# Kernel optimization log

Measured on AMD Instinct MI355X. Metric: run time of the kernel, lower is better.

The kernel has to match this reference:

```python
import jax, jax.numpy as jnp
import numpy as np

B, T, CODE_NUM, MED_NUM = 256, 32, 4880, 1000
CODE_SIZE, H, OUT = 128, 128, 4880


def setup_inputs() -> dict:
    key = jax.random.key(0)
    ks = jax.random.split(key, 16)
    code_x = (jax.random.uniform(ks[0], (B, T, CODE_NUM)) < 0.05).astype(jnp.float32)
    medicine_codes = (jax.random.uniform(ks[1], (B, T, MED_NUM)) < 0.02).astype(jnp.float32)
    divided = (jax.random.uniform(ks[2], (B, T, CODE_NUM)) < 0.05).astype(jnp.float32)
    neighbors = (jax.random.uniform(ks[3], (B, T, CODE_NUM)) < 0.05).astype(jnp.float32)
    lens = jax.random.randint(ks[4], (B,), 1, T + 1)
    s = lambda fan: 1.0 / np.sqrt(fan)
    c_emb = jax.random.normal(ks[5], (CODE_NUM, CODE_SIZE)) * s(CODE_SIZE)
    m_emb = jax.random.normal(ks[6], (MED_NUM, CODE_SIZE)) * s(CODE_SIZE)
    W_c = jax.random.normal(ks[7], (CODE_SIZE, H)) * s(CODE_SIZE)
    W_m = jax.random.normal(ks[8], (CODE_SIZE, H)) * s(CODE_SIZE)
    Wa = jax.random.normal(ks[9], (3 * H, 32)) * s(3 * H)
    ba = jnp.zeros((32,), jnp.float32)
    va = jax.random.normal(ks[10], (32,)) * s(32)
    W_cls = jax.random.normal(ks[11], (3 * H, OUT)) * s(3 * H)
    b_cls = jnp.zeros((OUT,), jnp.float32)
    return dict(code_x=code_x, divided=divided, neighbors=neighbors, lens=lens,
                medicine_codes=medicine_codes, c_emb=c_emb, m_emb=m_emb,
                W_c=W_c, W_m=W_m, Wa=Wa, ba=ba, va=va, W_cls=W_cls, b_cls=b_cls)


def _forward(code_x, medicine_codes, lens, c_emb, m_emb, W_c, W_m, Wa, ba, va, W_cls, b_cls):
    # hypergraph_part: transform code/med embeddings, aggregate active codes per visit
    Hc = jnp.tanh(c_emb @ W_c)                      # [code_num, H]
    Hm = jnp.tanh(m_emb @ W_m)                      # [med_num, H]
    sum_c = jnp.einsum('btc,ch->bth', code_x, Hc)   # masked sum over active dx codes
    sum_m = jnp.einsum('btm,mh->bth', medicine_codes, Hm)
    h_c = sum_c / jnp.clip(code_x.sum(-1, keepdims=True), 1.0, None)
    h_m = sum_m / jnp.clip(medicine_codes.sum(-1, keepdims=True), 1.0, None)
    repre = jnp.concatenate([h_c, h_m, h_c * h_m], axis=-1)  # [B,T,3H]
    # DotProductAttention over visits, masked by lens
    scores = jnp.einsum('btk,k->bt', jnp.tanh(repre @ Wa + ba), va)
    mask = jnp.arange(T)[None, :] < lens[:, None]
    attn = jax.nn.softmax(jnp.where(mask, scores, -1e9), axis=-1)
    ctx = jnp.einsum('bt,btd->bd', attn, repre)     # [B,3H]
    # Classifier (dropout=identity in eval) + sigmoid
    return jax.nn.sigmoid(ctx @ W_cls + b_cls)      # [B,OUT]


def reference(code_x, divided, neighbors, lens, medicine_codes, c_emb, m_emb,
              W_c, W_m, Wa, ba, va, W_cls, b_cls):
    # divided/neighbors feed the transition branch whose output is unused
    # in the original forward's final prediction path.
    return _forward(code_x, medicine_codes, lens, c_emb, m_emb,
                    W_c, W_m, Wa, ba, va, W_cls, b_cls)
```

## Files before the change

### kernel.cpp

```cpp
#include <hip/hip_runtime.h>
#include <hip/hip_bf16.h>
#include <math.h>

#define Bsz 256
#define Tn 32
#define CODEN 4880
#define MEDN 1000
#define Hdim 128
#define OUTN 4880
#define R3H 384
#define NROW (Bsz * Tn)
#define NC4 (CODEN / 4)
#define NM4 (MEDN / 4)
#define CCAP 384
#define MCAP 64
#define CROWS (CODEN + 8)
#define MROWS (MEDN + 8)

typedef unsigned short u16;
typedef unsigned int u32;
typedef __attribute__((ext_vector_type(4))) float f32x4;

__device__ inline int mbcnt64(unsigned long long m) {
  return __builtin_amdgcn_mbcnt_hi((u32)(m >> 32),
         __builtin_amdgcn_mbcnt_lo((u32)m, 0));
}
__device__ inline u32 f2bf(float f) {
  u32 u = __float_as_uint(f);
  return (u + 0x7fffu + ((u >> 16) & 1u)) >> 16;
}

__global__ __launch_bounds__(128) void k_emb(
    const float* __restrict__ c_emb, const float* __restrict__ m_emb,
    const float* __restrict__ W_c, const float* __restrict__ W_m,
    u32* __restrict__ Hc2, u32* __restrict__ Hm2) {
  int blk = blockIdx.x, h = threadIdx.x;
  bool is_med = blk >= CROWS;
  int c = is_med ? blk - CROWS : blk;
  int n = is_med ? MEDN : CODEN;
  u32* out2 = (is_med ? Hm2 + (size_t)c * 64 : Hc2 + (size_t)c * 64);
  if (c >= n) { if ((h & 1) == 0) out2[h >> 1] = 0; return; }
  const float* emb = (is_med ? m_emb : c_emb) + (size_t)c * Hdim;
  const float* W = is_med ? W_m : W_c;
  __shared__ float e[Hdim];
  e[h] = emb[h];
  __syncthreads();
  float acc = 0.f;
#pragma unroll 8
  for (int k = 0; k < Hdim; ++k) acc += e[k] * W[k * Hdim + h];
  float vme = tanhf(acc);
  float vnx = __shfl_down(vme, 1, 64);
  if ((h & 1) == 0) out2[h >> 1] = f2bf(vme) | (f2bf(vnx) << 16);
}

__global__ __launch_bounds__(256) void k_pack(
    const float* __restrict__ code_x, const float* __restrict__ med,
    u16* __restrict__ idx_c, u16* __restrict__ idx_m,
    int* __restrict__ cnt_c, int* __restrict__ cnt_m) {
  int v = blockIdx.x, tid = threadIdx.x, lane = tid & 63;
  __shared__ u16 lc[CCAP + 8];
  __shared__ u16 lm[MCAP + 8];
  __shared__ int cc, cm;
  if (tid == 0) { cc = 0; cm = 0; }
  __syncthreads();

  const float4* cx = (const float4*)(code_x + (size_t)v * CODEN);
  const float4* mx = (const float4*)(med + (size_t)v * MEDN);
  float4 x[5], xm;
#pragma unroll
  for (int it = 0; it < 5; ++it) {
    int i = it * 256 + tid;
    x[it] = (i < NC4) ? cx[i] : make_float4(0.f, 0.f, 0.f, 0.f);
  }
  xm = (tid < NM4) ? mx[tid] : make_float4(0.f, 0.f, 0.f, 0.f);

#pragma unroll
  for (int it = 0; it < 5; ++it) {
    int i = it * 256 + tid;
    float4 vv = x[it];
    unsigned long long m0 = __ballot(vv.x != 0.f);
    unsigned long long m1 = __ballot(vv.y != 0.f);
    unsigned long long m2 = __ballot(vv.z != 0.f);
    unsigned long long m3 = __ballot(vv.w != 0.f);
    int c0 = __popcll(m0), c1 = __popcll(m1), c2 = __popcll(m2), c3 = __popcll(m3);
    int base = 0;
    if (lane == 0) base = atomicAdd(&cc, c0 + c1 + c2 + c3);
    base = __builtin_amdgcn_readfirstlane(base);
    int p;
    p = base + mbcnt64(m0);             if (vv.x != 0.f && p < CCAP) lc[p] = (u16)(4 * i);
    p = base + c0 + mbcnt64(m1);        if (vv.y != 0.f && p < CCAP) lc[p] = (u16)(4 * i + 1);
    p = base + c0 + c1 + mbcnt64(m2);   if (vv.z != 0.f && p < CCAP) lc[p] = (u16)(4 * i + 2);
    p = base + c0 + c1 + c2 + mbcnt64(m3); if (vv.w != 0.f && p < CCAP) lc[p] = (u16)(4 * i + 3);
  }
  {
    int i = tid;
    unsigned long long m0 = __ballot(xm.x != 0.f);
    unsigned long long m1 = __ballot(xm.y != 0.f);
    unsigned long long m2 = __ballot(xm.z != 0.f);
    unsigned long long m3 = __ballot(xm.w != 0.f);
    int c0 = __popcll(m0), c1 = __popcll(m1), c2 = __popcll(m2), c3 = __popcll(m3);
    int base = 0;
    if (lane == 0) base = atomicAdd(&cm, c0 + c1 + c2 + c3);
    base = __builtin_amdgcn_readfirstlane(base);
    int p;
    p = base + mbcnt64(m0);             if (xm.x != 0.f && p < MCAP) lm[p] = (u16)(4 * i);
    p = base + c0 + mbcnt64(m1);        if (xm.y != 0.f && p < MCAP) lm[p] = (u16)(4 * i + 1);
    p = base + c0 + c1 + mbcnt64(m2);   if (xm.z != 0.f && p < MCAP) lm[p] = (u16)(4 * i + 2);
    p = base + c0 + c1 + c2 + mbcnt64(m3); if (xm.w != 0.f && p < MCAP) lm[p] = (u16)(4 * i + 3);
  }
  __syncthreads();
  int nc = cc < CCAP ? cc : CCAP;
  int nm = cm < MCAP ? cm : MCAP;
  int ncp = (nc + 7) & ~7, nmp = (nm + 7) & ~7;
  for (int i = nc + tid; i < ncp; i += 256) lc[i] = (u16)CODEN;
  for (int i = nm + tid; i < nmp; i += 256) lm[i] = (u16)MEDN;
  __syncthreads();
  u32* gc = (u32*)(idx_c + (size_t)v * CCAP);
  for (int i = tid; i < (ncp >> 1); i += 256) gc[i] = ((const u32*)lc)[i];
  u32* gm = (u32*)(idx_m + (size_t)v * MCAP);
  if (tid < (nmp >> 1)) gm[tid] = ((const u32*)lm)[tid];
  if (tid == 0) { cnt_c[v] = nc; cnt_m[v] = nm; }
}

__global__ __launch_bounds__(256) void k_gather(
    const u16* __restrict__ idx_c, const u16* __restrict__ idx_m,
    const int* __restrict__ cnt_c, const int* __restrict__ cnt_m,
    const u32* __restrict__ Hc2, const u32* __restrict__ Hm2,
    u32* __restrict__ rep2) {
  __shared__ u16 slc[4][CCAP];
  __shared__ u16 slm[4][MCAP];
  int tid = threadIdx.x;
  int w = tid >> 6, l = tid & 63;
  int v = blockIdx.x * 4 + w;
  int nc = cnt_c[v], nm = cnt_m[v];
  int ncp = (nc + 7) & ~7, nmp = (nm + 7) & ~7;

  {
    const u32* gc = (const u32*)(idx_c + (size_t)v * CCAP);
    u32* d = (u32*)slc[w];
    for (int i = l; i < (ncp >> 1); i += 64) d[i] = gc[i];
    const u32* gm = (const u32*)(idx_m + (size_t)v * MCAP);
    u32* dm = (u32*)slm[w];
    if (l < (nmp >> 1)) dm[l] = gm[l];
  }
  __syncthreads();

  float a0 = 0.f, a1 = 0.f;
  const u32* lcu = (const u32*)slc[w];
  for (int j = 0; j < ncp; j += 8) {
    u32 pr[4], vv[8];
#pragma unroll
    for (int u = 0; u < 4; ++u) pr[u] = lcu[(j >> 1) + u];
#pragma unroll
    for (int u = 0; u < 4; ++u) {
      vv[2 * u]     = Hc2[(size_t)(pr[u] & 0xffffu) * 64 + l];
      vv[2 * u + 1] = Hc2[(size_t)(pr[u] >> 16) * 64 + l];
    }
#pragma unroll
    for (int u = 0; u < 8; ++u) {
      a0 += __uint_as_float(vv[u] << 16);
      a1 += __uint_as_float(vv[u] & 0xffff0000u);
    }
  }
  float m0 = 0.f, m1 = 0.f;
  const u32* lmu = (const u32*)slm[w];
  for (int j = 0; j < nmp; j += 8) {
    u32 pr[4], vv[8];
#pragma unroll
    for (int u = 0; u < 4; ++u) pr[u] = lmu[(j >> 1) + u];
#pragma unroll
    for (int u = 0; u < 4; ++u) {
      vv[2 * u]     = Hm2[(size_t)(pr[u] & 0xffffu) * 64 + l];
      vv[2 * u + 1] = Hm2[(size_t)(pr[u] >> 16) * 64 + l];
    }
#pragma unroll
    for (int u = 0; u < 8; ++u) {
      m0 += __uint_as_float(vv[u] << 16);
      m1 += __uint_as_float(vv[u] & 0xffff0000u);
    }
  }
  float ic = 1.f / fmaxf((float)nc, 1.f);
  float im = 1.f / fmaxf((float)nm, 1.f);
  rep2[(size_t)v * 128 + l]      = f2bf(a0 * ic) | (f2bf(a1 * ic) << 16);
  rep2[(size_t)v * 128 + 64 + l] = f2bf(m0 * im) | (f2bf(m1 * im) << 16);
}

__global__ __launch_bounds__(256) void k_post(
    const u32* __restrict__ rep2, const float* __restrict__ Wa,
    const float* __restrict__ ba, const float* __restrict__ va,
    const int* __restrict__ lens, float* __restrict__ ctx) {
  __shared__ float rep_s[Tn][R3H + 4];
  __shared__ float sc_s[Tn];
  __shared__ float at_s[Tn];
  int b = blockIdx.x, tid = threadIdx.x;

  for (int i = tid; i < Tn * 128; i += 256) {
    int t = i >> 7, c = i & 127;
    u32 vv = rep2[(size_t)(b * Tn + t) * 128 + c];
    rep_s[t][2 * c]     = __uint_as_float(vv << 16);
    rep_s[t][2 * c + 1] = __uint_as_float(vv & 0xffff0000u);
  }
  __syncthreads();
  for (int i = tid; i < Tn * 128; i += 256) {
    int t = i >> 7, c = i & 127;
    rep_s[t][256 + c] = rep_s[t][c] * rep_s[t][128 + c];
  }
  __syncthreads();
  {
    int t = tid >> 3, j0 = (tid & 7) * 4;
    float u0 = 0.f, u1 = 0.f, u2 = 0.f, u3 = 0.f;
    for (int k = 0; k < R3H; ++k) {
      float r = rep_s[t][k];
      float4 wv = *(const float4*)(Wa + k * 32 + j0);
      u0 += r * wv.x; u1 += r * wv.y; u2 += r * wv.z; u3 += r * wv.w;
    }
    float sv = tanhf(u0 + ba[j0])     * va[j0]
             + tanhf(u1 + ba[j0 + 1]) * va[j0 + 1]
             + tanhf(u2 + ba[j0 + 2]) * va[j0 + 2]
             + tanhf(u3 + ba[j0 + 3]) * va[j0 + 3];
    sv += __shfl_xor(sv, 1, 64);
    sv += __shfl_xor(sv, 2, 64);
    sv += __shfl_xor(sv, 4, 64);
    if ((tid & 7) == 0) sc_s[t] = sv;
  }
  __syncthreads();
  if (tid < Tn) {
    int len = lens[b];
    float s = sc_s[tid];
    bool valid = tid < len;
    float sm = valid ? s : -1e30f;
    float m = sm;
#pragma unroll
    for (int off = 16; off >= 1; off >>= 1) m = fmaxf(m, __shfl_xor(m, off, 32));
    float e = valid ? expf(sm - m) : 0.f;
    float su = e;
#pragma unroll
    for (int off = 16; off >= 1; off >>= 1) su += __shfl_xor(su, off, 32);
    at_s[tid] = e / su;
  }
  __syncthreads();
  for (int d = tid; d < R3H; d += 256) {
    float a = 0.f;
#pragma unroll
    for (int t = 0; t < Tn; ++t) a += at_s[t] * rep_s[t][d];
    ctx[(size_t)b * R3H + d] = a;
  }
}

__device__ inline void fma4(float4& a, float s, const float4& w) {
  a.x += s * w.x; a.y += s * w.y; a.z += s * w.z; a.w += s * w.w;
}

__global__ __launch_bounds__(256) void k_cls(
    const float* __restrict__ ctx, const float* __restrict__ W_cls,
    const float* __restrict__ b_cls, float* __restrict__ out) {
  __shared__ float cs_t[R3H * 8];
  int tid = threadIdx.x;
  int ob = blockIdx.x % 5;
  int b0 = (blockIdx.x / 5) * 8;
  for (int i = tid; i < R3H * 8; i += 256) {
    int k = i >> 3, r = i & 7;
    cs_t[i] = ctx[(size_t)(b0 + r) * R3H + k];
  }
  __syncthreads();
  int o0 = ob * 1024 + tid * 4;
  if (o0 >= OUTN) return;
  float4 acc[8];
#pragma unroll
  for (int r = 0; r < 8; ++r) acc[r] = make_float4(0.f, 0.f, 0.f, 0.f);
  const float* wp = W_cls + o0;
  for (int k = 0; k < R3H; k += 8) {
    float4 wv[8];
#pragma unroll
    for (int u = 0; u < 8; ++u) wv[u] = *(const float4*)(wp + (size_t)(k + u) * OUTN);
#pragma unroll
    for (int u = 0; u < 8; ++u) {
      float4 cA = *(const float4*)&cs_t[(k + u) * 8];
      float4 cB = *(const float4*)&cs_t[(k + u) * 8 + 4];
      fma4(acc[0], cA.x, wv[u]); fma4(acc[1], cA.y, wv[u]);
      fma4(acc[2], cA.z, wv[u]); fma4(acc[3], cA.w, wv[u]);
      fma4(acc[4], cB.x, wv[u]); fma4(acc[5], cB.y, wv[u]);
      fma4(acc[6], cB.z, wv[u]); fma4(acc[7], cB.w, wv[u]);
    }
  }
  float4 bc = *(const float4*)(b_cls + o0);
#pragma unroll
  for (int r = 0; r < 8; ++r) {
    float4 v;
    v.x = 1.f / (1.f + expf(-(acc[r].x + bc.x)));
    v.y = 1.f / (1.f + expf(-(acc[r].y + bc.y)));
    v.z = 1.f / (1.f + expf(-(acc[r].z + bc.z)));
    v.w = 1.f / (1.f + expf(-(acc[r].w + bc.w)));
    *(float4*)(out + (size_t)(b0 + r) * OUTN + o0) = v;
  }
}

extern "C" void kernel_launch(void* const* d_in, const int* in_sizes, int n_in,
                              void* d_out, int out_size, void* d_ws, size_t ws_size,
                              hipStream_t stream) {
  const float* code_x = (const float*)d_in[0];
  const int*   lens   = (const int*)d_in[3];
  const float* med    = (const float*)d_in[4];
  const float* c_emb  = (const float*)d_in[5];
  const float* m_emb  = (const float*)d_in[6];
  const float* W_c    = (const float*)d_in[7];
  const float* W_m    = (const float*)d_in[8];
  const float* Wa     = (const float*)d_in[9];
  const float* ba     = (const float*)d_in[10];
  const float* va     = (const float*)d_in[11];
  const float* W_cls  = (const float*)d_in[12];
  const float* b_cls  = (const float*)d_in[13];
  float* out = (float*)d_out;

  u32* Hc2   = (u32*)d_ws;
  u32* Hm2   = Hc2 + (size_t)CROWS * 64;
  u32* rep2  = Hm2 + (size_t)MROWS * 64;
  u16* idx_c = (u16*)(rep2 + (size_t)NROW * 128);
  u16* idx_m = idx_c + (size_t)NROW * CCAP;
  int* cnt_c = (int*)(idx_m + (size_t)NROW * MCAP);
  int* cnt_m = cnt_c + NROW;
  float* ctx = (float*)(cnt_m + NROW);

  hipLaunchKernelGGL(k_emb, dim3(CROWS + MROWS), dim3(128), 0, stream,
                     c_emb, m_emb, W_c, W_m, Hc2, Hm2);
  hipLaunchKernelGGL(k_pack, dim3(NROW), dim3(256), 0, stream,
                     code_x, med, idx_c, idx_m, cnt_c, cnt_m);
  hipLaunchKernelGGL(k_gather, dim3(NROW / 4), dim3(256), 0, stream,
                     idx_c, idx_m, cnt_c, cnt_m, Hc2, Hm2, rep2);
  hipLaunchKernelGGL(k_post, dim3(Bsz), dim3(256), 0, stream,
                     rep2, Wa, ba, va, lens, ctx);
  hipLaunchKernelGGL(k_cls, dim3(160), dim3(256), 0, stream,
                     ctx, W_cls, b_cls, out);
}
```

Before: 549.0 us.

## Process four visits per pack block with prefetch; widen gather unroll to 16

The pack kernel now handles four visit rows per block and prefetches the next row's code and medicine data into registers while the current row is being compacted. This hides global load latency and cuts the block count. The gather loop now issues 16 independent row loads per iteration instead of 8, with padding and pad rows bumped to 16 to match. The cost is higher register pressure, fewer blocks in pack, and more padded dummy-row gathers.

```diff
diff --git a/kernel.cpp b/kernel.cpp
--- a/kernel.cpp
+++ b/kernel.cpp
@@ -14,8 +14,9 @@
 #define NM4 (MEDN / 4)
 #define CCAP 384
 #define MCAP 64
-#define CROWS (CODEN + 8)
-#define MROWS (MEDN + 8)
+#define CROWS (CODEN + 16)
+#define MROWS (MEDN + 16)
+#define VPB 4
 
 typedef unsigned short u16;
 typedef unsigned int u32;
@@ -53,73 +54,92 @@
   if ((h & 1) == 0) out2[h >> 1] = f2bf(vme) | (f2bf(vnx) << 16);
 }
 
+__device__ inline void loadV(const float* __restrict__ code_x,
+                             const float* __restrict__ med,
+                             int v, int tid, float4* x, float4& xm) {
+  const float4* cx = (const float4*)(code_x + (size_t)v * CODEN);
+#pragma unroll
+  for (int it = 0; it < 5; ++it) {
+    int i = it * 256 + tid;
+    x[it] = (i < NC4) ? cx[i] : make_float4(0.f, 0.f, 0.f, 0.f);
+  }
+  const float4* mx = (const float4*)(med + (size_t)v * MEDN);
+  xm = (tid < NM4) ? mx[tid] : make_float4(0.f, 0.f, 0.f, 0.f);
+}
+
 __global__ __launch_bounds__(256) void k_pack(
     const float* __restrict__ code_x, const float* __restrict__ med,
     u16* __restrict__ idx_c, u16* __restrict__ idx_m,
     int* __restrict__ cnt_c, int* __restrict__ cnt_m) {
-  int v = blockIdx.x, tid = threadIdx.x, lane = tid & 63;
-  __shared__ u16 lc[CCAP + 8];
-  __shared__ u16 lm[MCAP + 8];
+  int tid = threadIdx.x, lane = tid & 63;
+  __shared__ u16 lc[CCAP + 16];
+  __shared__ u16 lm[MCAP + 16];
   __shared__ int cc, cm;
-  if (tid == 0) { cc = 0; cm = 0; }
-  __syncthreads();
-
-  const float4* cx = (const float4*)(code_x + (size_t)v * CODEN);
-  const float4* mx = (const float4*)(med + (size_t)v * MEDN);
-  float4 x[5], xm;
-#pragma unroll
-  for (int it = 0; it < 5; ++it) {
-    int i = it * 256 + tid;
-    x[it] = (i < NC4) ? cx[i] : make_float4(0.f, 0.f, 0.f, 0.f);
-  }
-  xm = (tid < NM4) ? mx[tid] : make_float4(0.f, 0.f, 0.f, 0.f);
-
-#pragma unroll
-  for (int it = 0; it < 5; ++it) {
-    int i = it * 256 + tid;
-    float4 vv = x[it];
-    unsigned long long m0 = __ballot(vv.x != 0.f);
-    unsigned long long m1 = __ballot(vv.y != 0.f);
-    unsigned long long m2 = __ballot(vv.z != 0.f);
-    unsigned long long m3 = __ballot(vv.w != 0.f);
-    int c0 = __popcll(m0), c1 = __popcll(m1), c2 = __popcll(m2), c3 = __popcll(m3);
-    int base = 0;
-    if (lane == 0) base = atomicAdd(&cc, c0 + c1 + c2 + c3);
-    base = __builtin_amdgcn_readfirstlane(base);
-    int p;
-    p = base + mbcnt64(m0);             if (vv.x != 0.f && p < CCAP) lc[p] = (u16)(4 * i);
-    p = base + c0 + mbcnt64(m1);        if (vv.y != 0.f && p < CCAP) lc[p] = (u16)(4 * i + 1);
-    p = base + c0 + c1 + mbcnt64(m2);   if (vv.z != 0.f && p < CCAP) lc[p] = (u16)(4 * i + 2);
-    p = base + c0 + c1 + c2 + mbcnt64(m3); if (vv.w != 0.f && p < CCAP) lc[p] = (u16)(4 * i + 3);
-  }
-  {
-    int i = tid;
-    unsigned long long m0 = __ballot(xm.x != 0.f);
-    unsigned long long m1 = __ballot(xm.y != 0.f);
-    unsigned long long m2 = __ballot(xm.z != 0.f);
-    unsigned long long m3 = __ballot(xm.w != 0.f);
-    int c0 = __popcll(m0), c1 = __popcll(m1), c2 = __popcll(m2), c3 = __popcll(m3);
-    int base = 0;
-    if (lane == 0) base = atomicAdd(&cm, c0 + c1 + c2 + c3);
-    base = __builtin_amdgcn_readfirstlane(base);
-    int p;
-    p = base + mbcnt64(m0);             if (xm.x != 0.f && p < MCAP) lm[p] = (u16)(4 * i);
-    p = base + c0 + mbcnt64(m1);        if (xm.y != 0.f && p < MCAP) lm[p] = (u16)(4 * i + 1);
-    p = base + c0 + c1 + mbcnt64(m2);   if (xm.z != 0.f && p < MCAP) lm[p] = (u16)(4 * i + 2);
-    p = base + c0 + c1 + c2 + mbcnt64(m3); if (xm.w != 0.f && p < MCAP) lm[p] = (u16)(4 * i + 3);
-  }
-  __syncthreads();
-  int nc = cc < CCAP ? cc : CCAP;
-  int nm = cm < MCAP ? cm : MCAP;
-  int ncp = (nc + 7) & ~7, nmp = (nm + 7) & ~7;
-  for (int i = nc + tid; i < ncp; i += 256) lc[i] = (u16)CODEN;
-  for (int i = nm + tid; i < nmp; i += 256) lm[i] = (u16)MEDN;
-  __syncthreads();
-  u32* gc = (u32*)(idx_c + (size_t)v * CCAP);
-  for (int i = tid; i < (ncp >> 1); i += 256) gc[i] = ((const u32*)lc)[i];
-  u32* gm = (u32*)(idx_m + (size_t)v * MCAP);
-  if (tid < (nmp >> 1)) gm[tid] = ((const u32*)lm)[tid];
-  if (tid == 0) { cnt_c[v] = nc; cnt_m[v] = nm; }
+  int v0 = blockIdx.x * VPB;
+
+  float4 xc[5], xn[5], mc, mn;
+  loadV(code_x, med, v0, tid, xc, mc);
+
+  for (int dv = 0; dv < VPB; ++dv) {
+    int v = v0 + dv;
+    if (tid == 0) { cc = 0; cm = 0; }
+    __syncthreads();
+    if (dv + 1 < VPB) loadV(code_x, med, v + 1, tid, xn, mn);
+
+#pragma unroll
+    for (int it = 0; it < 5; ++it) {
+      int i = it * 256 + tid;
+      float4 vv = xc[it];
+      unsigned long long m0 = __ballot(vv.x != 0.f);
+      unsigned long long m1 = __ballot(vv.y != 0.f);
+      unsigned long long m2 = __ballot(vv.z != 0.f);
+      unsigned long long m3 = __ballot(vv.w != 0.f);
+      int c0 = __popcll(m0), c1 = __popcll(m1), c2 = __popcll(m2), c3 = __popcll(m3);
+      int base = 0;
+      if (lane == 0) base = atomicAdd(&cc, c0 + c1 + c2 + c3);
+      base = __builtin_amdgcn_readfirstlane(base);
+      int p;
+      p = base + mbcnt64(m0);                if (vv.x != 0.f && p < CCAP) lc[p] = (u16)(4 * i);
+      p = base + c0 + mbcnt64(m1);           if (vv.y != 0.f && p < CCAP) lc[p] = (u16)(4 * i + 1);
+      p = base + c0 + c1 + mbcnt64(m2);      if (vv.z != 0.f && p < CCAP) lc[p] = (u16)(4 * i + 2);
+      p = base + c0 + c1 + c2 + mbcnt64(m3); if (vv.w != 0.f && p < CCAP) lc[p] = (u16)(4 * i + 3);
+    }
+    {
+      int i = tid;
+      float4 vv = mc;
+      unsigned long long m0 = __ballot(vv.x != 0.f);
+      unsigned long long m1 = __ballot(vv.y != 0.f);
+      unsigned long long m2 = __ballot(vv.z != 0.f);
+      unsigned long long m3 = __ballot(vv.w != 0.f);
+      int c0 = __popcll(m0), c1 = __popcll(m1), c2 = __popcll(m2), c3 = __popcll(m3);
+      int base = 0;
+      if (lane == 0) base = atomicAdd(&cm, c0 + c1 + c2 + c3);
+      base = __builtin_amdgcn_readfirstlane(base);
+      int p;
+      p = base + mbcnt64(m0);                if (vv.x != 0.f && p < MCAP) lm[p] = (u16)(4 * i);
+      p = base + c0 + mbcnt64(m1);           if (vv.y != 0.f && p < MCAP) lm[p] = (u16)(4 * i + 1);
+      p = base + c0 + c1 + mbcnt64(m2);      if (vv.z != 0.f && p < MCAP) lm[p] = (u16)(4 * i + 2);
+      p = base + c0 + c1 + c2 + mbcnt64(m3); if (vv.w != 0.f && p < MCAP) lm[p] = (u16)(4 * i + 3);
+    }
+    __syncthreads();
+    int nc = cc < CCAP ? cc : CCAP;
+    int nm = cm < MCAP ? cm : MCAP;
+    int ncp = (nc + 15) & ~15, nmp = (nm + 15) & ~15;
+    for (int i = nc + tid; i < ncp; i += 256) lc[i] = (u16)CODEN;
+    for (int i = nm + tid; i < nmp; i += 256) lm[i] = (u16)MEDN;
+    __syncthreads();
+    u32* gc = (u32*)(idx_c + (size_t)v * CCAP);
+    for (int i = tid; i < (ncp >> 1); i += 256) gc[i] = ((const u32*)lc)[i];
+    u32* gm = (u32*)(idx_m + (size_t)v * MCAP);
+    if (tid < (nmp >> 1)) gm[tid] = ((const u32*)lm)[tid];
+    if (tid == 0) { cnt_c[v] = nc; cnt_m[v] = nm; }
+
+    if (dv + 1 < VPB) {
+#pragma unroll
+      for (int it = 0; it < 5; ++it) xc[it] = xn[it];
+      mc = mn;
+    }
+  }
 }
 
 __global__ __launch_bounds__(256) void k_gather(
@@ -133,7 +153,7 @@
   int w = tid >> 6, l = tid & 63;
   int v = blockIdx.x * 4 + w;
   int nc = cnt_c[v], nm = cnt_m[v];
-  int ncp = (nc + 7) & ~7, nmp = (nm + 7) & ~7;
+  int ncp = (nc + 15) & ~15, nmp = (nm + 15) & ~15;
 
   {
     const u32* gc = (const u32*)(idx_c + (size_t)v * CCAP);
@@ -147,34 +167,34 @@
 
   float a0 = 0.f, a1 = 0.f;
   const u32* lcu = (const u32*)slc[w];
-  for (int j = 0; j < ncp; j += 8) {
-    u32 pr[4], vv[8];
-#pragma unroll
-    for (int u = 0; u < 4; ++u) pr[u] = lcu[(j >> 1) + u];
-#pragma unroll
-    for (int u = 0; u < 4; ++u) {
+  for (int j = 0; j < ncp; j += 16) {
+    u32 pr[8], vv[16];
+#pragma unroll
+    for (int u = 0; u < 8; ++u) pr[u] = lcu[(j >> 1) + u];
+#pragma unroll
+    for (int u = 0; u < 8; ++u) {
       vv[2 * u]     = Hc2[(size_t)(pr[u] & 0xffffu) * 64 + l];
       vv[2 * u + 1] = Hc2[(size_t)(pr[u] >> 16) * 64 + l];
     }
 #pragma unroll
-    for (int u = 0; u < 8; ++u) {
+    for (int u = 0; u < 16; ++u) {
       a0 += __uint_as_float(vv[u] << 16);
       a1 += __uint_as_float(vv[u] & 0xffff0000u);
     }
   }
   float m0 = 0.f, m1 = 0.f;
   const u32* lmu = (const u32*)slm[w];
-  for (int j = 0; j < nmp; j += 8) {
-    u32 pr[4], vv[8];
-#pragma unroll
-    for (int u = 0; u < 4; ++u) pr[u] = lmu[(j >> 1) + u];
-#pragma unroll
-    for (int u = 0; u < 4; ++u) {
+  for (int j = 0; j < nmp; j += 16) {
+    u32 pr[8], vv[16];
+#pragma unroll
+    for (int u = 0; u < 8; ++u) pr[u] = lmu[(j >> 1) + u];
+#pragma unroll
+    for (int u = 0; u < 8; ++u) {
       vv[2 * u]     = Hm2[(size_t)(pr[u] & 0xffffu) * 64 + l];
       vv[2 * u + 1] = Hm2[(size_t)(pr[u] >> 16) * 64 + l];
     }
 #pragma unroll
-    for (int u = 0; u < 8; ++u) {
+    for (int u = 0; u < 16; ++u) {
       m0 += __uint_as_float(vv[u] << 16);
       m1 += __uint_as_float(vv[u] & 0xffff0000u);
     }
@@ -323,7 +343,7 @@
 
   hipLaunchKernelGGL(k_emb, dim3(CROWS + MROWS), dim3(128), 0, stream,
                      c_emb, m_emb, W_c, W_m, Hc2, Hm2);
-  hipLaunchKernelGGL(k_pack, dim3(NROW), dim3(256), 0, stream,
+  hipLaunchKernelGGL(k_pack, dim3(NROW / VPB), dim3(256), 0, stream,
                      code_x, med, idx_c, idx_m, cnt_c, cnt_m);
   hipLaunchKernelGGL(k_gather, dim3(NROW / 4), dim3(256), 0, stream,
                      idx_c, idx_m, cnt_c, cnt_m, Hc2, Hm2, rep2);
```

New measurement: 552.0 us. Within noise of the previous version (+0.5%).
